# Kernel tuning notes

Hardware: AMD Instinct MI355X
Metric: run time of the kernel (lower is better)

Reference implementation:

```python
import jax, jax.numpy as jnp
import numpy as np

B, T, E, H = 4, 2048, 1024, 16
D = E // H
PAD_TOKEN_ID = 0
VOCAB = 50257


def setup_inputs() -> dict:
    key = jax.random.key(0)
    k1, k2, k3, k4 = jax.random.split(key, 4)
    x = jax.random.normal(k1, (B, T, E), dtype=jnp.float32)
    input_ids = jax.random.randint(k2, (B, T), 0, VOCAB, dtype=jnp.int64)
    # guarantee first key of every sequence is non-pad so no softmax row is fully masked
    input_ids = input_ids.at[:, 0].set(1)
    w_qkv = jax.random.normal(k3, (E, 3 * E), dtype=jnp.float32) * 0.02
    w_out = jax.random.normal(k4, (E, E), dtype=jnp.float32) * 0.02
    b_out = jnp.zeros((E,), dtype=jnp.float32)
    return {"x": x, "input_ids": input_ids, "w_qkv": w_qkv, "w_out": w_out, "b_out": b_out}


def reference(x, input_ids, w_qkv, w_out, b_out):
    b, t, e = x.shape
    # fused QKV projection (bias=False in original)
    qkv = x @ w_qkv                                   # [B,T,3E]
    q, k, v = jnp.split(qkv, 3, axis=-1)
    q = q.reshape(b, t, H, D).transpose(0, 2, 1, 3)   # [B,H,T,D]
    k = k.reshape(b, t, H, D).transpose(0, 2, 1, 3)
    v = v.reshape(b, t, H, D).transpose(0, 2, 1, 3)

    scale = 1.0 / jnp.sqrt(jnp.asarray(D, dtype=x.dtype))
    scores = jnp.einsum("bhqd,bhkd->bhqk", q, k) * scale   # [B,H,T,T]

    causal = jnp.tril(jnp.ones((t, t), dtype=bool))         # [T,T]
    key_keep = (input_ids != PAD_TOKEN_ID)[:, None, None, :]  # [B,1,1,T]
    mask = causal[None, None, :, :] & key_keep               # [B,1(T broadcast over H),T,T]
    scores = jnp.where(mask, scores, -jnp.inf)

    attn = jax.nn.softmax(scores, axis=-1)                   # dropout_p=0 in eval
    y = jnp.einsum("bhqk,bhkd->bhqd", attn, v)               # [B,H,T,D]
    y = y.transpose(0, 2, 1, 3).reshape(b, t, e)             # [B,T,E]
    return y @ w_out + b_out
```

## Files before the change

### kernel.cpp

```cpp
#include <hip/hip_runtime.h>
#include <hip/hip_bf16.h>
#include <stdint.h>

#define Hn 16
#define Tn 2048
#define En 1024
#define Dh 64

typedef __bf16 bf16x8 __attribute__((ext_vector_type(8)));
typedef float f32x4 __attribute__((ext_vector_type(4)));
typedef unsigned short u16;
typedef u16 u16x8 __attribute__((ext_vector_type(8)));

#define SCALE_Q 0.18033688f

__device__ __forceinline__ u16 f2bf(float f) {
  union { float f; uint32_t u; } v; v.f = f;
  uint32_t r = v.u + 0x7fffu + ((v.u >> 16) & 1u);
  return (u16)(r >> 16);
}

typedef const __attribute__((address_space(1))) void gvoid_t;
typedef __attribute__((address_space(3))) void lvoid_t;
__device__ __forceinline__ void gl_lds16(const void* g, void* l) {
  __builtin_amdgcn_global_load_lds((gvoid_t*)g, (lvoid_t*)l, 16, 0, 0);
}

__global__ void cvt_x_k(const float* __restrict__ in, u16* __restrict__ out) {
  int i = (blockIdx.x * 256 + threadIdx.x) * 8;
  float4 a = *(const float4*)(in + i);
  float4 b = *(const float4*)(in + i + 4);
  u16x8 o;
  o[0] = f2bf(a.x); o[1] = f2bf(a.y); o[2] = f2bf(a.z); o[3] = f2bf(a.w);
  o[4] = f2bf(b.x); o[5] = f2bf(b.y); o[6] = f2bf(b.z); o[7] = f2bf(b.w);
  *(u16x8*)(out + i) = o;
}

__global__ void transpose_cvt_k(const float* __restrict__ in, u16* __restrict__ out,
                                int R, int C) {
  __shared__ float tile[32][33];
  int c0 = blockIdx.x * 32, r0 = blockIdx.y * 32;
  for (int i = threadIdx.y; i < 32; i += 8)
    tile[i][threadIdx.x] = in[(size_t)(r0 + i) * C + c0 + threadIdx.x];
  __syncthreads();
  for (int i = threadIdx.y; i < 32; i += 8)
    out[(size_t)(c0 + i) * R + r0 + threadIdx.x] = f2bf(tile[threadIdx.x][i]);
}

__global__ void prep_mask_k(const int* __restrict__ in, float* __restrict__ maskf) {
  __shared__ int is64_s;
  if (threadIdx.x == 0) {
    int all0 = 1;
    for (int i = 1; i < 256; i += 2) all0 &= (in[i] == 0);
    is64_s = all0;
  }
  __syncthreads();
  int i = blockIdx.x * 256 + threadIdx.x;
  int v = is64_s ? in[2 * i] : in[i];
  maskf[i] = (v != 0) ? 0.f : -1e30f;
}

__device__ __forceinline__ void gemm_mainloop(const u16* __restrict__ A,
                                              const u16* __restrict__ Bt,
                                              int K, int m0, int n0,
                                              u16* lds, f32x4 acc[4][4]) {
  const int tid = threadIdx.x;
  const int lane = tid & 63;
  const int w = tid >> 6;
  const int wm = (w >> 1) * 64, wn = (w & 1) * 64;
  const int quad = lane >> 4, ln = lane & 15;

  const int e0 = w * 512 + lane * 8;
  const int r0 = e0 >> 5, c0 = e0 & 31;

  const u16* gA0 = A + (size_t)(m0 + r0) * K + c0;
  const u16* gA1 = gA0 + (size_t)64 * K;
  const u16* gB0 = Bt + (size_t)(n0 + r0) * K + c0;
  const u16* gB1 = gB0 + (size_t)64 * K;
  u16* lA0 = lds + e0;
  u16* lA1 = lds + e0 + 2048;
  u16* lB0 = lds + e0 + 4096;
  u16* lB1 = lds + e0 + 6144;

  for (int k0 = 0; k0 < K; k0 += 32) {
    gl_lds16(gA0 + k0, lA0);
    gl_lds16(gA1 + k0, lA1);
    gl_lds16(gB0 + k0, lB0);
    gl_lds16(gB1 + k0, lB1);
    __syncthreads();
    bf16x8 af[4], bfr[4];
#pragma unroll
    for (int mt = 0; mt < 4; mt++)
      af[mt] = *(const bf16x8*)(lds + (wm + mt * 16 + ln) * 32 + quad * 8);
#pragma unroll
    for (int nt = 0; nt < 4; nt++)
      bfr[nt] = *(const bf16x8*)(lds + 4096 + (wn + nt * 16 + ln) * 32 + quad * 8);
#pragma unroll
    for (int mt = 0; mt < 4; mt++)
#pragma unroll
      for (int nt = 0; nt < 4; nt++)
        acc[mt][nt] = __builtin_amdgcn_mfma_f32_16x16x32_bf16(af[mt], bfr[nt],
                                                              acc[mt][nt], 0, 0, 0);
    __syncthreads();
  }
}

__global__ __launch_bounds__(256, 3)
void gemm_qkv_kernel(const u16* __restrict__ X, const u16* __restrict__ Wt,
                     u16* __restrict__ Qo, u16* __restrict__ Ko,
                     u16* __restrict__ Vto) {
  __shared__ __align__(16) u16 lds[128 * 130];
  const int m0 = blockIdx.y * 128, n0 = blockIdx.x * 128;
  f32x4 acc[4][4];
#pragma unroll
  for (int i = 0; i < 4; i++)
#pragma unroll
    for (int j = 0; j < 4; j++) acc[i][j] = (f32x4){0.f, 0.f, 0.f, 0.f};

  gemm_mainloop(X, Wt, En, m0, n0, lds, acc);

  const int tid = threadIdx.x, lane = tid & 63, w = tid >> 6;
  const int wm = (w >> 1) * 64, wn = (w & 1) * 64;
  const int quad = lane >> 4, ln = lane & 15;
  const int which = n0 >> 10;
  const int bb = m0 >> 11, t0 = m0 & (Tn - 1);

  if (which < 2) {
#pragma unroll
    for (int mt = 0; mt < 4; mt++)
#pragma unroll
      for (int nt = 0; nt < 4; nt++)
#pragma unroll
        for (int r = 0; r < 4; r++) {
          int t = t0 + wm + mt * 16 + quad * 4 + r;
          int ng = n0 + wn + nt * 16 + ln;
          int e = ng & (En - 1);
          int h = e >> 6, d = e & 63;
          size_t bh = (size_t)(bb * Hn + h);
          if (which == 0)
            Qo[(bh * Tn + t) * Dh + d] = f2bf(acc[mt][nt][r] * SCALE_Q);
          else
            Ko[(bh * Tn + t) * Dh + d] = f2bf(acc[mt][nt][r]);
        }
  } else {
#pragma unroll
    for (int mt = 0; mt < 4; mt++)
#pragma unroll
      for (int nt = 0; nt < 4; nt++)
#pragma unroll
        for (int r = 0; r < 4; r++)
          lds[(wm + mt * 16 + quad * 4 + r) * 130 + wn + nt * 16 + ln] =
              f2bf(acc[mt][nt][r]);
    __syncthreads();
    const int ebase = n0 & (En - 1);
#pragma unroll
    for (int i = 0; i < 32; i++) {
      int col = w * 32 + i;
      int e = ebase + col;
      int hh = e >> 6, d = e & 63;
      size_t vrow = (((size_t)(bb * Hn + hh)) * Dh + d) * Tn + t0;
      Vto[vrow + lane] = lds[lane * 130 + col];
      Vto[vrow + 64 + lane] = lds[(64 + lane) * 130 + col];
    }
  }
}

__global__ __launch_bounds__(256, 3)
void gemm_out_kernel(const u16* __restrict__ Y, const u16* __restrict__ Wt,
                     const float* __restrict__ bias, float* __restrict__ Out) {
  __shared__ __align__(16) u16 lds[8192];
  const int m0 = blockIdx.y * 128, n0 = blockIdx.x * 128;
  f32x4 acc[4][4];
#pragma unroll
  for (int i = 0; i < 4; i++)
#pragma unroll
    for (int j = 0; j < 4; j++) acc[i][j] = (f32x4){0.f, 0.f, 0.f, 0.f};

  gemm_mainloop(Y, Wt, En, m0, n0, lds, acc);

  const int tid = threadIdx.x, lane = tid & 63, w = tid >> 6;
  const int wm = (w >> 1) * 64, wn = (w & 1) * 64;
  const int quad = lane >> 4, ln = lane & 15;

#pragma unroll
  for (int mt = 0; mt < 4; mt++)
#pragma unroll
    for (int nt = 0; nt < 4; nt++)
#pragma unroll
      for (int r = 0; r < 4; r++) {
        int mg = m0 + wm + mt * 16 + quad * 4 + r;
        int ng = n0 + wn + nt * 16 + ln;
        Out[(size_t)mg * En + ng] = acc[mt][nt][r] + bias[ng];
      }
}

__global__ __launch_bounds__(256, 3)
void attn_kernel(const u16* __restrict__ Q, const u16* __restrict__ K,
                 const u16* __restrict__ Vt, const float* __restrict__ maskf,
                 u16* __restrict__ Y) {
  __shared__ __align__(16) u16 Pl[128 * 76];

  const int bid = blockIdx.x;
  const int g = bid >> 8, sq = (bid >> 6) & 3;
  int qt;
  if (g == 0)      qt = 15 - sq;
  else if (g == 1) qt = sq;
  else if (g == 2) qt = 11 - sq;
  else             qt = 4 + sq;
  const int bh = bid & 63;
  const int b = bh >> 4, h = bh & 15;
  const int tid = threadIdx.x, lane = tid & 63, w = tid >> 6;
  const int quad = lane >> 4, ln = lane & 15;
  const int qb = w * 32;
  const int g0 = qt * 128 + qb;

  const size_t baseQK = (size_t)bh * (Tn * Dh);
  const size_t baseV = (size_t)bh * (Dh * Tn);
  const float* mrow = maskf + b * Tn;

  bf16x8 aq[2][2];
#pragma unroll
  for (int rt = 0; rt < 2; rt++)
#pragma unroll
    for (int ks = 0; ks < 2; ks++)
      aq[rt][ks] = *(const bf16x8*)(Q + baseQK +
          (size_t)(g0 + rt * 16 + ln) * Dh + ks * 32 + quad * 8);

  f32x4 O[2][4];
  float lsum[2][4];
#pragma unroll
  for (int rt = 0; rt < 2; rt++) {
#pragma unroll
    for (int dt = 0; dt < 4; dt++) O[rt][dt] = (f32x4){0.f, 0.f, 0.f, 0.f};
#pragma unroll
    for (int r = 0; r < 4; r++) lsum[rt][r] = 0.f;
  }

  auto tile = [&](int k0, bool dg) {
    f32x4 s[2][4];
    {
      bf16x8 bk[4][2];
      float kvf[4];
#pragma unroll
      for (int ct = 0; ct < 4; ct++) {
        kvf[ct] = mrow[k0 + ct * 16 + ln];
#pragma unroll
        for (int ks = 0; ks < 2; ks++)
          bk[ct][ks] = *(const bf16x8*)(K + baseQK +
              (size_t)(k0 + ct * 16 + ln) * Dh + ks * 32 + quad * 8);
      }
#pragma unroll
      for (int rt = 0; rt < 2; rt++)
#pragma unroll
        for (int ct = 0; ct < 4; ct++)
          s[rt][ct] = (f32x4){kvf[ct], kvf[ct], kvf[ct], kvf[ct]};
      __builtin_amdgcn_s_setprio(1);
#pragma unroll
      for (int ks = 0; ks < 2; ks++)
#pragma unroll
        for (int rt = 0; rt < 2; rt++)
#pragma unroll
          for (int ct = 0; ct < 4; ct++)
            s[rt][ct] = __builtin_amdgcn_mfma_f32_16x16x32_bf16(aq[rt][ks], bk[ct][ks],
                                                                s[rt][ct], 0, 0, 0);
      __builtin_amdgcn_s_setprio(0);
    }

    bf16x8 bv[4][2];
#pragma unroll
    for (int dt = 0; dt < 4; dt++)
#pragma unroll
      for (int ks = 0; ks < 2; ks++)
        bv[dt][ks] = *(const bf16x8*)(Vt + baseV +
            (size_t)(dt * 16 + ln) * Tn + k0 + ks * 32 + quad * 8);

#pragma unroll
    for (int rt = 0; rt < 2; rt++) {
      if (dg) {
#pragma unroll
        for (int ct = 0; ct < 4; ct++)
#pragma unroll
          for (int r = 0; r < 4; r++) {
            int qg = g0 + rt * 16 + quad * 4 + r;
            int kg = k0 + ct * 16 + ln;
            float v = (kg > qg) ? -1e30f : s[rt][ct][r];
            float p = exp2f(fminf(v, 126.f));
            lsum[rt][r] += p;
            Pl[(qb + rt * 16 + quad * 4 + r) * 76 + ct * 16 + ln] = f2bf(p);
          }
      } else {
#pragma unroll
        for (int ct = 0; ct < 4; ct++)
#pragma unroll
          for (int r = 0; r < 4; r++) {
            float p = exp2f(fminf(s[rt][ct][r], 126.f));
            lsum[rt][r] += p;
            Pl[(qb + rt * 16 + quad * 4 + r) * 76 + ct * 16 + ln] = f2bf(p);
          }
      }
    }

    __builtin_amdgcn_s_setprio(1);
#pragma unroll
    for (int ks2 = 0; ks2 < 2; ks2++)
#pragma unroll
      for (int rt = 0; rt < 2; rt++) {
        bf16x8 ap = *(const bf16x8*)(Pl + (qb + rt * 16 + ln) * 76 + ks2 * 32 + quad * 8);
#pragma unroll
        for (int dt = 0; dt < 4; dt++)
          O[rt][dt] = __builtin_amdgcn_mfma_f32_16x16x32_bf16(ap, bv[dt][ks2],
                                                              O[rt][dt], 0, 0, 0);
      }
    __builtin_amdgcn_s_setprio(0);
  };

  const int nfull = g0 >> 6;
  for (int kt = 0; kt < nfull; kt++) tile(kt * 64, false);
  tile(nfull * 64, true);

#pragma unroll
  for (int rt = 0; rt < 2; rt++)
#pragma unroll
    for (int r = 0; r < 4; r++) {
      float l = lsum[rt][r];
#pragma unroll
      for (int off = 1; off < 16; off <<= 1) l += __shfl_xor(l, off);
      float inv = 1.f / l;
      int tg = g0 + rt * 16 + quad * 4 + r;
      size_t ob = ((size_t)b * Tn + tg) * En + h * Dh;
#pragma unroll
      for (int dt = 0; dt < 4; dt++)
        Y[ob + dt * 16 + ln] = f2bf(O[rt][dt][r] * inv);
    }
}

#define OFF_MASK  0
#define OFF_WQKVT 16384
#define OFF_WOUTT (OFF_WQKVT + 3145728)
#define OFF_Q     (OFF_WOUTT + 1048576)
#define OFF_K     (OFF_Q + 8388608)
#define OFF_XY    (OFF_K + 8388608)

extern "C" void kernel_launch(void* const* d_in, const int* in_sizes, int n_in,
                              void* d_out, int out_size, void* d_ws, size_t ws_size,
                              hipStream_t stream) {
  const float* x = nullptr;
  const int* ids_raw = nullptr;
  const float* wqkv = nullptr;
  const float* wout = nullptr;
  const float* bias = nullptr;
  for (int i = 0; i < n_in; i++) {
    switch (in_sizes[i]) {
      case 8388608: x = (const float*)d_in[i]; break;
      case 8192:    ids_raw = (const int*)d_in[i]; break;
      case 3145728: wqkv = (const float*)d_in[i]; break;
      case 1048576: wout = (const float*)d_in[i]; break;
      case 1024:    bias = (const float*)d_in[i]; break;
      default: break;
    }
  }
  if (!x) x = (const float*)d_in[0];
  if (!ids_raw) ids_raw = (const int*)d_in[1];
  if (!wqkv) wqkv = (const float*)d_in[2];
  if (!wout) wout = (const float*)d_in[3];
  if (!bias) bias = (const float*)d_in[4];

  u16* ws = (u16*)d_ws;
  float* maskf = (float*)(ws + OFF_MASK);
  u16* wqkv_t = ws + OFF_WQKVT;
  u16* wout_t = ws + OFF_WOUTT;
  u16* Qb = ws + OFF_Q;
  u16* Kb = ws + OFF_K;
  u16* XbYb = ws + OFF_XY;
  u16* Vtb = (u16*)d_out;
  float* out = (float*)d_out;

  prep_mask_k<<<32, 256, 0, stream>>>(ids_raw, maskf);
  cvt_x_k<<<4096, 256, 0, stream>>>(x, XbYb);
  transpose_cvt_k<<<dim3(96, 32), dim3(32, 8), 0, stream>>>(wqkv, wqkv_t, 1024, 3072);
  transpose_cvt_k<<<dim3(32, 32), dim3(32, 8), 0, stream>>>(wout, wout_t, 1024, 1024);
  gemm_qkv_kernel<<<dim3(24, 64), 256, 0, stream>>>(XbYb, wqkv_t, Qb, Kb, Vtb);
  attn_kernel<<<1024, 256, 0, stream>>>(Qb, Kb, Vtb, maskf, XbYb);
  gemm_out_kernel<<<dim3(8, 64), 256, 0, stream>>>(XbYb, wout_t, bias, out);
}
```

Measured before the change: 327.9 us.

## Stage K tiles through double-buffered swizzled LDS with async global-to-LDS loads

K tiles are now brought into a two-slot shared-memory buffer through direct global-to-LDS loads issued by the whole block. The next tile is prefetched while the current one is processed, and an XOR swizzle avoids bank conflicts. This replaces per-wave direct global reads of K, which were duplicated across the four waves, with one shared copy and overlapped loading. In exchange it adds 16KB of LDS, which may lower occupancy under launch_bounds(256,3), and a __syncthreads every iteration. Waves whose diagonal tile comes earlier now sit idle through the extra iterations.

```diff
diff --git a/kernel.cpp b/kernel.cpp
--- a/kernel.cpp
+++ b/kernel.cpp
@@ -199,6 +199,7 @@
                  const u16* __restrict__ Vt, const float* __restrict__ maskf,
                  u16* __restrict__ Y) {
   __shared__ __align__(16) u16 Pl[128 * 76];
+  __shared__ __align__(16) u16 KL[2 * 4096];
 
   const int bid = blockIdx.x;
   const int g = bid >> 8, sq = (bid >> 6) & 3;
@@ -217,6 +218,19 @@
   const size_t baseQK = (size_t)bh * (Tn * Dh);
   const size_t baseV = (size_t)bh * (Dh * Tn);
   const float* mrow = maskf + b * Tn;
+  const u16* Kp = K + baseQK;
+
+  const int srow = tid >> 3;
+  const int scol = ((tid & 7) * 8) ^ ((srow & 7) * 8);
+  const u16* gK0 = Kp + (size_t)srow * Dh + scol;
+  const u16* gK1 = Kp + (size_t)(srow + 32) * Dh + scol;
+  u16* lK0 = KL + tid * 8;
+  u16* lK1 = lK0 + 2048;
+
+  auto stage = [&](int buf, int k0) {
+    gl_lds16(gK0 + (size_t)k0 * Dh, lK0 + buf * 4096);
+    gl_lds16(gK1 + (size_t)k0 * Dh, lK1 + buf * 4096);
+  };
 
   bf16x8 aq[2][2];
 #pragma unroll
@@ -236,7 +250,7 @@
     for (int r = 0; r < 4; r++) lsum[rt][r] = 0.f;
   }
 
-  auto tile = [&](int k0, bool dg) {
+  auto tile = [&](const u16* kl, int k0, bool dg) {
     f32x4 s[2][4];
     {
       bf16x8 bk[4][2];
@@ -246,8 +260,8 @@
         kvf[ct] = mrow[k0 + ct * 16 + ln];
 #pragma unroll
         for (int ks = 0; ks < 2; ks++)
-          bk[ct][ks] = *(const bf16x8*)(K + baseQK +
-              (size_t)(k0 + ct * 16 + ln) * Dh + ks * 32 + quad * 8);
+          bk[ct][ks] = *(const bf16x8*)(kl + (ct * 16 + ln) * 64 +
+                                        ((ks * 32 + quad * 8) ^ ((ln & 7) * 8)));
       }
 #pragma unroll
       for (int rt = 0; rt < 2; rt++)
@@ -315,8 +329,16 @@
   };
 
   const int nfull = g0 >> 6;
-  for (int kt = 0; kt < nfull; kt++) tile(kt * 64, false);
-  tile(nfull * 64, true);
+  const int NT = 2 * qt + 1;
+  stage(0, 0);
+  int cur = 0;
+  for (int kt = 0; kt <= NT; kt++) {
+    __syncthreads();
+    if (kt < NT) stage(cur ^ 1, (kt + 1) * 64);
+    if (kt < nfull)       tile(KL + cur * 4096, kt * 64, false);
+    else if (kt == nfull) tile(KL + cur * 4096, kt * 64, true);
+    cur ^= 1;
+  }
 
 #pragma unroll
   for (int rt = 0; rt < 2; rt++)
```

Measured after the change: 288.3 us. 1.14x faster.
